# Optimization experiments

Measured on AMD Instinct MI355X. Metric: run time of the kernel, lower is better.

Reference implementation:

```python
import jax, jax.numpy as jnp
import numpy as np

B, LQ, LS, H = 4, 4096, 4096, 1024

def setup_inputs() -> dict:
    key = jax.random.key(0)
    k1, k2 = jax.random.split(key)
    query_input = jax.random.normal(k1, (B, LQ, H), dtype=jnp.float32)
    source_input = jax.random.normal(k2, (B, LS, H), dtype=jnp.float32)
    return {"query_input": query_input, "source_input": source_input}

def reference(query_input, source_input):
    # logits: [B, LQ, LS] = Q @ S^T, scaled by sqrt(d_k)
    dk = jnp.asarray(query_input.shape[-1], dtype=query_input.dtype)
    logits = jnp.einsum('bqh,bsh->bqs', query_input, source_input) / jnp.sqrt(dk)
    weights = jax.nn.softmax(logits, axis=-1)  # dropout inactive in eval mode
    # output: [B, LQ, H] = weights @ S (source doubles as values)
    return jnp.einsum('bqs,bsh->bqh', weights, source_input)
```

## Files before the change

### kernel.cpp

```cpp
#include <hip/hip_runtime.h>
#include <hip/hip_bf16.h>

#define B_   4
#define LQ_  4096
#define LS_  4096
#define DH_  1024
#define BQ_  64
#define BS_  256
#define NT_  (LS_/BS_)
#define NTH  512

typedef __bf16 bf16x8 __attribute__((ext_vector_type(8)));
typedef float  f32x4  __attribute__((ext_vector_type(4)));
typedef float  f32x16 __attribute__((ext_vector_type(16)));
typedef unsigned char u8;

#define WAITL()  asm volatile("s_waitcnt lgkmcnt(0)" ::: "memory")
#define BAR()    __builtin_amdgcn_s_barrier()

__device__ __forceinline__ unsigned short f2bf(float f) {
  union { __bf16 h; unsigned short u; } cv;
  cv.h = (__bf16)f;
  return cv.u;
}
__device__ __forceinline__ bf16x8 cvt8(f32x4 a, f32x4 b) {
  bf16x8 r;
  r[0] = (__bf16)a[0]; r[1] = (__bf16)a[1]; r[2] = (__bf16)a[2]; r[3] = (__bf16)a[3];
  r[4] = (__bf16)b[0]; r[5] = (__bf16)b[1]; r[6] = (__bf16)b[2]; r[7] = (__bf16)b[3];
  return r;
}

__global__ __launch_bounds__(256) void cvt_kernel(const float* __restrict__ S,
                                                  u8* __restrict__ Kf,
                                                  u8* __restrict__ Vf)
{
  __shared__ unsigned short tile[64][72];
  const int b  = blockIdx.z;
  const int dt = blockIdx.y;
  const int st = blockIdx.x;
  const int tid = threadIdx.x;
  const int t  = st >> 2;
  const float* Sbase = S + ((size_t)b*LS_ + (size_t)st*64)*DH_ + dt*64;

  #pragma unroll
  for (int k = 0; k < 4; ++k) {
    int fi  = tid + k*256;
    int row = fi >> 4;
    int c4  = fi & 15;
    float4 v = *reinterpret_cast<const float4*>(Sbase + (size_t)row*DH_ + c4*4);
    ushort4 h;
    h.x = f2bf(v.x); h.y = f2bf(v.y); h.z = f2bf(v.z); h.w = f2bf(v.w);
    *reinterpret_cast<ushort4*>(&tile[row][c4*4]) = h;
  }
  __syncthreads();

  #pragma unroll
  for (int h2 = 0; h2 < 2; ++h2) {
    int u    = tid + h2*256;
    int blk  = u >> 6;
    int wloc = blk >> 2;
    int kkl  = blk & 3;
    int lane = u & 63;
    int sh   = lane >> 5, sl = lane & 31;
    int srow = wloc*32 + sl;
    int scol = kkl*16 + sh*8;
    ushort4 h0 = *reinterpret_cast<const ushort4*>(&tile[srow][scol]);
    ushort4 h1 = *reinterpret_cast<const ushort4*>(&tile[srow][scol+4]);
    int w_g  = (st & 3)*2 + wloc;
    int kk_g = dt*4 + kkl;
    u8* dst = Kf + (size_t)(((b*16 + t)*8 + w_g)*64 + kk_g)*1024 + lane*16;
    *reinterpret_cast<ushort4*>(dst)     = h0;
    *reinterpret_cast<ushort4*>(dst + 8) = h1;
  }

  #pragma unroll
  for (int h2 = 0; h2 < 2; ++h2) {
    int u    = tid + h2*256;
    int blk  = u >> 6;
    int ksl  = blk >> 2;
    int nfl  = blk & 3;
    int lane = u & 63;
    int lg   = lane >> 4, lr = lane & 15;
    int srow = ksl*32 + lg*8;
    int dcol = nfl*16 + lr;
    ushort4 h0, h1;
    h0.x = tile[srow+0][dcol]; h0.y = tile[srow+1][dcol];
    h0.z = tile[srow+2][dcol]; h0.w = tile[srow+3][dcol];
    h1.x = tile[srow+4][dcol]; h1.y = tile[srow+5][dcol];
    h1.z = tile[srow+6][dcol]; h1.w = tile[srow+7][dcol];
    int w_g = dt >> 1;
    int i_g = ((st & 3)*2 + ksl)*8 + (dt & 1)*4 + nfl;
    u8* dst = Vf + (size_t)(((b*16 + t)*8 + w_g)*64 + i_g)*1024 + lane*16;
    *reinterpret_cast<ushort4*>(dst)     = h0;
    *reinterpret_cast<ushort4*>(dst + 8) = h1;
  }
}

__global__ __launch_bounds__(NTH, 1) void attn_kernel(
    const float* __restrict__ Qg,
    const u8* __restrict__ Kf,
    const u8* __restrict__ Vf,
    float* __restrict__ Og)
{
  __shared__ __align__(16) unsigned char qlds[131072];
  __shared__ __align__(16) unsigned char plds[32768];

  const int tid = threadIdx.x;
  const int w  = tid >> 6;
  const int l  = tid & 63;
  const int lg = l >> 4;
  const int lr = l & 15;
  const int sl = l & 31;
  const int sh = l >> 5;

  const int n    = blockIdx.x;
  const int xcd  = n & 7;
  const int slot = n >> 3;
  const int b    = xcd >> 1;
  const int qt   = (xcd & 1)*32 + slot;

  const float* Qbase = Qg + ((size_t)b*LQ_ + (size_t)qt*BQ_)*DH_;
  const u8* kptr = Kf + (size_t)b*8388608 + (size_t)w*65536 + l*16;
  const u8* vptr = Vf + (size_t)b*8388608 + (size_t)w*65536 + l*16;

  bf16x8 bk[4];
  auto ld_bk = [&](int t, int kk) -> bf16x8 {
    return *reinterpret_cast<const bf16x8*>(kptr + (size_t)t*524288 + kk*1024);
  };
  bf16x8 bv[4];
  auto ld_bv = [&](int t, int i) -> bf16x8 {
    return *reinterpret_cast<const bf16x8*>(vptr + (size_t)t*524288 + i*1024);
  };
  auto ldP = [&](int mq, int ks) -> bf16x8 {
    int q = mq*16 + lr;
    return *reinterpret_cast<const bf16x8*>(
        plds + q*512 + ((ks*64 + lg*16) ^ ((q & 7) << 4)));
  };

  bk[0] = ld_bk(0, 0); bk[1] = ld_bk(0, 1); bk[2] = ld_bk(0, 2);

  #pragma unroll
  for (int it = 0; it < 16; ++it) {
    int u  = tid + it*NTH;
    int qf = u >> 12;
    int kk = (u >> 6) & 63;
    int ll = u & 63;
    int q  = qf*32 + (ll & 31);
    int d  = kk*16 + (ll >> 5)*8;
    const float* p = Qbase + (size_t)q*DH_ + d;
    f32x4 v0 = *reinterpret_cast<const f32x4*>(p);
    f32x4 v1 = *reinterpret_cast<const f32x4*>(p + 4);
    *reinterpret_cast<bf16x8*>(qlds + (size_t)u*16) = cvt8(v0, v1);
  }

  f32x4 Oacc[4][8];
  #pragma unroll
  for (int i = 0; i < 4; ++i)
    #pragma unroll
    for (int j = 0; j < 8; ++j)
      Oacc[i][j] = (f32x4){0.f, 0.f, 0.f, 0.f};
  f32x4 lacc[4];
  #pragma unroll
  for (int i = 0; i < 4; ++i) lacc[i] = (f32x4){0.f, 0.f, 0.f, 0.f};

  bf16x8 ones;
  #pragma unroll
  for (int e = 0; e < 8; ++e) ones[e] = (__bf16)1.0f;

  f32x16 qk0, qk1;
  const float SCL = 0.04508422f;

  WAITL();
  BAR();

  #pragma unroll
  for (int r = 0; r < 16; ++r) { qk0[r] = 0.f; qk1[r] = 0.f; }
  {
    bf16x8 aqA0 = *reinterpret_cast<const bf16x8*>(qlds + l*16);
    bf16x8 aqA1 = *reinterpret_cast<const bf16x8*>(qlds + 65536 + l*16);
    #pragma unroll
    for (int kk = 0; kk < 64; ++kk) {
      if (kk < 61) bk[(kk + 3) & 3] = ld_bk(0, kk + 3);
      bf16x8 aqN0, aqN1;
      if (kk < 63) {
        aqN0 = *reinterpret_cast<const bf16x8*>(qlds + (kk + 1)*1024 + l*16);
        aqN1 = *reinterpret_cast<const bf16x8*>(qlds + 65536 + (kk + 1)*1024 + l*16);
      }
      qk0 = __builtin_amdgcn_mfma_f32_32x32x16_bf16(aqA0, bk[kk & 3], qk0, 0, 0, 0);
      qk1 = __builtin_amdgcn_mfma_f32_32x32x16_bf16(aqA1, bk[kk & 3], qk1, 0, 0, 0);
      if (kk < 63) { aqA0 = aqN0; aqA1 = aqN1; }
    }
  }

  for (int t = 1; t < NT_; ++t) {
    BAR();

    #pragma unroll
    for (int r = 0; r < 16; ++r) {
      int qrow = (r & 3) + 8*(r >> 2) + 4*sh;
      int s    = w*32 + sl;
      {
        float p = exp2f(qk0[r] * SCL);
        int q = qrow;
        *reinterpret_cast<__bf16*>(plds + q*512 + ((s*2) ^ ((q & 7) << 4))) = (__bf16)p;
      }
      {
        float p = exp2f(qk1[r] * SCL);
        int q = 32 + qrow;
        *reinterpret_cast<__bf16*>(plds + q*512 + ((s*2) ^ ((q & 7) << 4))) = (__bf16)p;
      }
    }

    bk[0] = ld_bk(t, 0); bk[1] = ld_bk(t, 1); bk[2] = ld_bk(t, 2);
    bv[0] = ld_bv(t-1, 0); bv[1] = ld_bv(t-1, 1); bv[2] = ld_bv(t-1, 2);

    WAITL();
    BAR();

    #pragma unroll
    for (int r = 0; r < 16; ++r) { qk0[r] = 0.f; qk1[r] = 0.f; }

    bf16x8 aqA0 = *reinterpret_cast<const bf16x8*>(qlds + l*16);
    bf16x8 aqA1 = *reinterpret_cast<const bf16x8*>(qlds + 65536 + l*16);
    bf16x8 pa0, pa1, pa2, pa3;

    #pragma unroll
    for (int i = 0; i < 64; ++i) {
      const int ks = i >> 3, nf = i & 7;
      if (i < 61) bk[(i + 3) & 3] = ld_bk(t, i + 3);
      bf16x8 aqN0, aqN1;
      if (i < 63) {
        aqN0 = *reinterpret_cast<const bf16x8*>(qlds + (i + 1)*1024 + l*16);
        aqN1 = *reinterpret_cast<const bf16x8*>(qlds + 65536 + (i + 1)*1024 + l*16);
      }
      qk0 = __builtin_amdgcn_mfma_f32_32x32x16_bf16(aqA0, bk[i & 3], qk0, 0, 0, 0);
      qk1 = __builtin_amdgcn_mfma_f32_32x32x16_bf16(aqA1, bk[i & 3], qk1, 0, 0, 0);
      if (i < 63) { aqA0 = aqN0; aqA1 = aqN1; }

      if (i < 61) bv[(i + 3) & 3] = ld_bv(t-1, i + 3);
      if (nf == 0) {
        pa0 = ldP(0, ks); pa1 = ldP(1, ks); pa2 = ldP(2, ks); pa3 = ldP(3, ks);
        if (w == 0) {
          lacc[0] = __builtin_amdgcn_mfma_f32_16x16x32_bf16(pa0, ones, lacc[0], 0, 0, 0);
          lacc[1] = __builtin_amdgcn_mfma_f32_16x16x32_bf16(pa1, ones, lacc[1], 0, 0, 0);
          lacc[2] = __builtin_amdgcn_mfma_f32_16x16x32_bf16(pa2, ones, lacc[2], 0, 0, 0);
          lacc[3] = __builtin_amdgcn_mfma_f32_16x16x32_bf16(pa3, ones, lacc[3], 0, 0, 0);
        }
      }
      Oacc[0][nf] = __builtin_amdgcn_mfma_f32_16x16x32_bf16(pa0, bv[i & 3], Oacc[0][nf], 0, 0, 0);
      Oacc[1][nf] = __builtin_amdgcn_mfma_f32_16x16x32_bf16(pa1, bv[i & 3], Oacc[1][nf], 0, 0, 0);
      Oacc[2][nf] = __builtin_amdgcn_mfma_f32_16x16x32_bf16(pa2, bv[i & 3], Oacc[2][nf], 0, 0, 0);
      Oacc[3][nf] = __builtin_amdgcn_mfma_f32_16x16x32_bf16(pa3, bv[i & 3], Oacc[3][nf], 0, 0, 0);
    }
  }

  BAR();
  #pragma unroll
  for (int r = 0; r < 16; ++r) {
    int qrow = (r & 3) + 8*(r >> 2) + 4*sh;
    int s    = w*32 + sl;
    {
      float p = exp2f(qk0[r] * SCL);
      int q = qrow;
      *reinterpret_cast<__bf16*>(plds + q*512 + ((s*2) ^ ((q & 7) << 4))) = (__bf16)p;
    }
    {
      float p = exp2f(qk1[r] * SCL);
      int q = 32 + qrow;
      *reinterpret_cast<__bf16*>(plds + q*512 + ((s*2) ^ ((q & 7) << 4))) = (__bf16)p;
    }
  }
  bv[0] = ld_bv(NT_-1, 0); bv[1] = ld_bv(NT_-1, 1); bv[2] = ld_bv(NT_-1, 2);
  WAITL();
  BAR();

  {
    bf16x8 pa0, pa1, pa2, pa3;
    #pragma unroll
    for (int i = 0; i < 64; ++i) {
      const int ks = i >> 3, nf = i & 7;
      if (i < 61) bv[(i + 3) & 3] = ld_bv(NT_-1, i + 3);
      if (nf == 0) {
        pa0 = ldP(0, ks); pa1 = ldP(1, ks); pa2 = ldP(2, ks); pa3 = ldP(3, ks);
        if (w == 0) {
          lacc[0] = __builtin_amdgcn_mfma_f32_16x16x32_bf16(pa0, ones, lacc[0], 0, 0, 0);
          lacc[1] = __builtin_amdgcn_mfma_f32_16x16x32_bf16(pa1, ones, lacc[1], 0, 0, 0);
          lacc[2] = __builtin_amdgcn_mfma_f32_16x16x32_bf16(pa2, ones, lacc[2], 0, 0, 0);
          lacc[3] = __builtin_amdgcn_mfma_f32_16x16x32_bf16(pa3, ones, lacc[3], 0, 0, 0);
        }
      }
      Oacc[0][nf] = __builtin_amdgcn_mfma_f32_16x16x32_bf16(pa0, bv[i & 3], Oacc[0][nf], 0, 0, 0);
      Oacc[1][nf] = __builtin_amdgcn_mfma_f32_16x16x32_bf16(pa1, bv[i & 3], Oacc[1][nf], 0, 0, 0);
      Oacc[2][nf] = __builtin_amdgcn_mfma_f32_16x16x32_bf16(pa2, bv[i & 3], Oacc[2][nf], 0, 0, 0);
      Oacc[3][nf] = __builtin_amdgcn_mfma_f32_16x16x32_bf16(pa3, bv[i & 3], Oacc[3][nf], 0, 0, 0);
    }
  }
  BAR();

  float* lred = (float*)plds;
  if (w == 0 && lr == 0) {
    #pragma unroll
    for (int mq = 0; mq < 4; ++mq)
      #pragma unroll
      for (int j = 0; j < 4; ++j)
        lred[mq*16 + lg*4 + j] = lacc[mq][j];
  }
  WAITL();
  BAR();

  float* Ob = Og + ((size_t)b*LQ_ + (size_t)qt*BQ_)*DH_;
  #pragma unroll
  for (int mq = 0; mq < 4; ++mq)
    #pragma unroll
    for (int j = 0; j < 4; ++j) {
      int q = mq*16 + lg*4 + j;
      float rinv = 1.0f / lred[q];
      #pragma unroll
      for (int nf = 0; nf < 8; ++nf)
        Ob[(size_t)q*DH_ + w*128 + nf*16 + lr] = Oacc[mq][nf][j] * rinv;
    }
}

__global__ void attn_naive(const float* __restrict__ Q, const float* __restrict__ S,
                           float* __restrict__ O)
{
  const int row = blockIdx.x;
  const int b = row >> 12, q = row & 4095;
  const float* qp = Q + ((size_t)b*LQ_ + q)*DH_;
  const float* sp = S + (size_t)b*LS_*DH_;
  __shared__ float qs[DH_];
  __shared__ float osum[DH_];
  __shared__ float lsum;
  for (int i = threadIdx.x; i < DH_; i += 256) { qs[i] = qp[i]; osum[i] = 0.f; }
  if (threadIdx.x == 0) lsum = 0.f;
  __syncthreads();
  float lpart = 0.f;
  for (int s0 = threadIdx.x; s0 < LS_; s0 += 256) {
    const float* sr = sp + (size_t)s0*DH_;
    float dot = 0.f;
    for (int d = 0; d < DH_; ++d) dot += qs[d]*sr[d];
    float p = __expf(dot * 0.03125f);
    lpart += p;
    for (int d = 0; d < DH_; ++d) atomicAdd(&osum[d], p*sr[d]);
  }
  atomicAdd(&lsum, lpart);
  __syncthreads();
  float rinv = 1.0f / lsum;
  float* op = O + ((size_t)b*LQ_ + q)*DH_;
  for (int i = threadIdx.x; i < DH_; i += 256) op[i] = osum[i]*rinv;
}

extern "C" void kernel_launch(void* const* d_in, const int* in_sizes, int n_in,
                              void* d_out, int out_size, void* d_ws, size_t ws_size,
                              hipStream_t stream)
{
  const float* Q = (const float*)d_in[0];
  const float* S = (const float*)d_in[1];
  float* out = (float*)d_out;

  const size_t kf_bytes = (size_t)B_*NT_*8*64*1024;
  const size_t vf_bytes = (size_t)B_*NT_*8*64*1024;
  const size_t need = kf_bytes + vf_bytes;

  if (ws_size >= need) {
    u8* Kf = (u8*)d_ws;
    u8* Vf = Kf + kf_bytes;
    cvt_kernel<<<dim3(64, 16, 4), 256, 0, stream>>>(S, Kf, Vf);
    attn_kernel<<<dim3(256), NTH, 0, stream>>>(Q, Kf, Vf, out);
  } else {
    attn_naive<<<dim3(B_*LQ_), 256, 0, stream>>>(Q, S, out);
  }
}
```

Measured before the change: 347.7 us.

## Stagger K/V chunk order per block and rotate row-sum work across waves

The inner 64-step loops are split into 8 segments of 8. Each block starts at a different segment offset derived from its slot, so concurrent blocks read different parts of K/V at any moment. K/V prefetch now runs continuously across tile boundaries using a 4-deep register rotation, which removes the reload at the start of each tile, and s_setprio is raised around the MFMA groups. The row-sum MFMA work is spread across waves (the wave whose index matches the segment does it) instead of always running on wave 0, with a final cross-wave reduction through LDS. The segment loops use unroll 1, which adds loop overhead and dynamic index math in exchange for smaller code.

```diff
diff --git a/kernel.cpp b/kernel.cpp
--- a/kernel.cpp
+++ b/kernel.cpp
@@ -118,26 +118,27 @@
   const int slot = n >> 3;
   const int b    = xcd >> 1;
   const int qt   = (xcd & 1)*32 + slot;
+  const int off  = slot & 7;
 
   const float* Qbase = Qg + ((size_t)b*LQ_ + (size_t)qt*BQ_)*DH_;
   const u8* kptr = Kf + (size_t)b*8388608 + (size_t)w*65536 + l*16;
   const u8* vptr = Vf + (size_t)b*8388608 + (size_t)w*65536 + l*16;
 
-  bf16x8 bk[4];
-  auto ld_bk = [&](int t, int kk) -> bf16x8 {
-    return *reinterpret_cast<const bf16x8*>(kptr + (size_t)t*524288 + kk*1024);
-  };
-  bf16x8 bv[4];
-  auto ld_bv = [&](int t, int i) -> bf16x8 {
-    return *reinterpret_cast<const bf16x8*>(vptr + (size_t)t*524288 + i*1024);
+  bf16x8 bk[4], bv[4];
+  auto ldU = [&](const u8* base, int unit) -> bf16x8 {
+    return *reinterpret_cast<const bf16x8*>(base + unit*1024);
   };
   auto ldP = [&](int mq, int ks) -> bf16x8 {
     int q = mq*16 + lr;
     return *reinterpret_cast<const bf16x8*>(
         plds + q*512 + ((ks*64 + lg*16) ^ ((q & 7) << 4)));
   };
-
-  bk[0] = ld_bk(0, 0); bk[1] = ld_bk(0, 1); bk[2] = ld_bk(0, 2);
+  auto ldA = [&](int kk, int qf) -> bf16x8 {
+    return *reinterpret_cast<const bf16x8*>(qlds + qf*65536 + kk*1024 + l*16);
+  };
+
+  bk[0] = ldU(kptr, off*8 + 0); bk[1] = ldU(kptr, off*8 + 1);
+  bk[2] = ldU(kptr, off*8 + 2); bk[3] = ldU(kptr, off*8 + 3);
 
   #pragma unroll
   for (int it = 0; it < 16; ++it) {
@@ -173,25 +174,35 @@
   WAITL();
   BAR();
 
+  bf16x8 aqA0 = ldA(off*8, 0);
+  bf16x8 aqA1 = ldA(off*8, 1);
+
   #pragma unroll
   for (int r = 0; r < 16; ++r) { qk0[r] = 0.f; qk1[r] = 0.f; }
-  {
-    bf16x8 aqA0 = *reinterpret_cast<const bf16x8*>(qlds + l*16);
-    bf16x8 aqA1 = *reinterpret_cast<const bf16x8*>(qlds + 65536 + l*16);
-    #pragma unroll
-    for (int kk = 0; kk < 64; ++kk) {
-      if (kk < 61) bk[(kk + 3) & 3] = ld_bk(0, kk + 3);
-      bf16x8 aqN0, aqN1;
-      if (kk < 63) {
-        aqN0 = *reinterpret_cast<const bf16x8*>(qlds + (kk + 1)*1024 + l*16);
-        aqN1 = *reinterpret_cast<const bf16x8*>(qlds + 65536 + (kk + 1)*1024 + l*16);
+  #pragma unroll 1
+  for (int seg = 0; seg < 8; ++seg) {
+    const int ibe = (seg + off) & 7;
+    const int ibn = (ibe + 1) & 7;
+    const u8* kP = (seg < 7) ? kptr : kptr + 524288;
+    #pragma unroll
+    for (int j = 0; j < 8; ++j) {
+      const int nu = (j < 7) ? (ibe*8 + j + 1) : (ibn*8);
+      bf16x8 aqN0 = ldA(nu, 0);
+      bf16x8 aqN1 = ldA(nu, 1);
+      __builtin_amdgcn_s_setprio(1);
+      qk0 = __builtin_amdgcn_mfma_f32_32x32x16_bf16(aqA0, bk[j & 3], qk0, 0, 0, 0);
+      qk1 = __builtin_amdgcn_mfma_f32_32x32x16_bf16(aqA1, bk[j & 3], qk1, 0, 0, 0);
+      __builtin_amdgcn_s_setprio(0);
+      if (j < 4) bk[j] = ldU(kptr, ibe*8 + j + 4);
+      else {
+        bk[j - 4] = ldU(kP, ibn*8 + j - 4);
+        if (seg == 7) bv[j - 4] = ldU(vptr, ibn*8 + j - 4);
       }
-      qk0 = __builtin_amdgcn_mfma_f32_32x32x16_bf16(aqA0, bk[kk & 3], qk0, 0, 0, 0);
-      qk1 = __builtin_amdgcn_mfma_f32_32x32x16_bf16(aqA1, bk[kk & 3], qk1, 0, 0, 0);
-      if (kk < 63) { aqA0 = aqN0; aqA1 = aqN1; }
-    }
-  }
-
+      aqA0 = aqN0; aqA1 = aqN1;
+    }
+  }
+
+  #pragma unroll 1
   for (int t = 1; t < NT_; ++t) {
     BAR();
 
@@ -210,47 +221,53 @@
         *reinterpret_cast<__bf16*>(plds + q*512 + ((s*2) ^ ((q & 7) << 4))) = (__bf16)p;
       }
     }
-
-    bk[0] = ld_bk(t, 0); bk[1] = ld_bk(t, 1); bk[2] = ld_bk(t, 2);
-    bv[0] = ld_bv(t-1, 0); bv[1] = ld_bv(t-1, 1); bv[2] = ld_bv(t-1, 2);
-
     WAITL();
     BAR();
 
     #pragma unroll
     for (int r = 0; r < 16; ++r) { qk0[r] = 0.f; qk1[r] = 0.f; }
 
-    bf16x8 aqA0 = *reinterpret_cast<const bf16x8*>(qlds + l*16);
-    bf16x8 aqA1 = *reinterpret_cast<const bf16x8*>(qlds + 65536 + l*16);
+    const u8* kT = kptr + (size_t)t*524288;
+    const u8* vT = vptr + (size_t)(t-1)*524288;
     bf16x8 pa0, pa1, pa2, pa3;
 
-    #pragma unroll
-    for (int i = 0; i < 64; ++i) {
-      const int ks = i >> 3, nf = i & 7;
-      if (i < 61) bk[(i + 3) & 3] = ld_bk(t, i + 3);
-      bf16x8 aqN0, aqN1;
-      if (i < 63) {
-        aqN0 = *reinterpret_cast<const bf16x8*>(qlds + (i + 1)*1024 + l*16);
-        aqN1 = *reinterpret_cast<const bf16x8*>(qlds + 65536 + (i + 1)*1024 + l*16);
+    #pragma unroll 1
+    for (int seg = 0; seg < 8; ++seg) {
+      const int ibe = (seg + off) & 7;
+      const int ibn = (ibe + 1) & 7;
+      const u8* kP = (seg < 7) ? kT : kT + 524288;
+      const u8* vP = (seg < 7) ? vT : vT + 524288;
+      #pragma unroll
+      for (int j = 0; j < 8; ++j) {
+        const int nu = (j < 7) ? (ibe*8 + j + 1) : (ibn*8);
+        bf16x8 aqN0 = ldA(nu, 0);
+        bf16x8 aqN1 = ldA(nu, 1);
+        if (j == 0) {
+          pa0 = ldP(0, ibe); pa1 = ldP(1, ibe); pa2 = ldP(2, ibe); pa3 = ldP(3, ibe);
+          if (ibe == w) {
+            lacc[0] = __builtin_amdgcn_mfma_f32_16x16x32_bf16(pa0, ones, lacc[0], 0, 0, 0);
+            lacc[1] = __builtin_amdgcn_mfma_f32_16x16x32_bf16(pa1, ones, lacc[1], 0, 0, 0);
+            lacc[2] = __builtin_amdgcn_mfma_f32_16x16x32_bf16(pa2, ones, lacc[2], 0, 0, 0);
+            lacc[3] = __builtin_amdgcn_mfma_f32_16x16x32_bf16(pa3, ones, lacc[3], 0, 0, 0);
+          }
+        }
+        __builtin_amdgcn_s_setprio(1);
+        qk0 = __builtin_amdgcn_mfma_f32_32x32x16_bf16(aqA0, bk[j & 3], qk0, 0, 0, 0);
+        qk1 = __builtin_amdgcn_mfma_f32_32x32x16_bf16(aqA1, bk[j & 3], qk1, 0, 0, 0);
+        Oacc[0][j] = __builtin_amdgcn_mfma_f32_16x16x32_bf16(pa0, bv[j & 3], Oacc[0][j], 0, 0, 0);
+        Oacc[1][j] = __builtin_amdgcn_mfma_f32_16x16x32_bf16(pa1, bv[j & 3], Oacc[1][j], 0, 0, 0);
+        Oacc[2][j] = __builtin_amdgcn_mfma_f32_16x16x32_bf16(pa2, bv[j & 3], Oacc[2][j], 0, 0, 0);
+        Oacc[3][j] = __builtin_amdgcn_mfma_f32_16x16x32_bf16(pa3, bv[j & 3], Oacc[3][j], 0, 0, 0);
+        __builtin_amdgcn_s_setprio(0);
+        if (j < 4) {
+          bk[j] = ldU(kT, ibe*8 + j + 4);
+          bv[j] = ldU(vT, ibe*8 + j + 4);
+        } else {
+          bk[j - 4] = ldU(kP, ibn*8 + j - 4);
+          bv[j - 4] = ldU(vP, ibn*8 + j - 4);
+        }
+        aqA0 = aqN0; aqA1 = aqN1;
       }
-      qk0 = __builtin_amdgcn_mfma_f32_32x32x16_bf16(aqA0, bk[i & 3], qk0, 0, 0, 0);
-      qk1 = __builtin_amdgcn_mfma_f32_32x32x16_bf16(aqA1, bk[i & 3], qk1, 0, 0, 0);
-      if (i < 63) { aqA0 = aqN0; aqA1 = aqN1; }
-
-      if (i < 61) bv[(i + 3) & 3] = ld_bv(t-1, i + 3);
-      if (nf == 0) {
-        pa0 = ldP(0, ks); pa1 = ldP(1, ks); pa2 = ldP(2, ks); pa3 = ldP(3, ks);
-        if (w == 0) {
-          lacc[0] = __builtin_amdgcn_mfma_f32_16x16x32_bf16(pa0, ones, lacc[0], 0, 0, 0);
-          lacc[1] = __builtin_amdgcn_mfma_f32_16x16x32_bf16(pa1, ones, lacc[1], 0, 0, 0);
-          lacc[2] = __builtin_amdgcn_mfma_f32_16x16x32_bf16(pa2, ones, lacc[2], 0, 0, 0);
-          lacc[3] = __builtin_amdgcn_mfma_f32_16x16x32_bf16(pa3, ones, lacc[3], 0, 0, 0);
-        }
-      }
-      Oacc[0][nf] = __builtin_amdgcn_mfma_f32_16x16x32_bf16(pa0, bv[i & 3], Oacc[0][nf], 0, 0, 0);
-      Oacc[1][nf] = __builtin_amdgcn_mfma_f32_16x16x32_bf16(pa1, bv[i & 3], Oacc[1][nf], 0, 0, 0);
-      Oacc[2][nf] = __builtin_amdgcn_mfma_f32_16x16x32_bf16(pa2, bv[i & 3], Oacc[2][nf], 0, 0, 0);
-      Oacc[3][nf] = __builtin_amdgcn_mfma_f32_16x16x32_bf16(pa3, bv[i & 3], Oacc[3][nf], 0, 0, 0);
     }
   }
 
@@ -270,40 +287,47 @@
       *reinterpret_cast<__bf16*>(plds + q*512 + ((s*2) ^ ((q & 7) << 4))) = (__bf16)p;
     }
   }
-  bv[0] = ld_bv(NT_-1, 0); bv[1] = ld_bv(NT_-1, 1); bv[2] = ld_bv(NT_-1, 2);
   WAITL();
   BAR();
 
   {
+    const u8* vT = vptr + (size_t)(NT_-1)*524288;
     bf16x8 pa0, pa1, pa2, pa3;
-    #pragma unroll
-    for (int i = 0; i < 64; ++i) {
-      const int ks = i >> 3, nf = i & 7;
-      if (i < 61) bv[(i + 3) & 3] = ld_bv(NT_-1, i + 3);
-      if (nf == 0) {
-        pa0 = ldP(0, ks); pa1 = ldP(1, ks); pa2 = ldP(2, ks); pa3 = ldP(3, ks);
-        if (w == 0) {
-          lacc[0] = __builtin_amdgcn_mfma_f32_16x16x32_bf16(pa0, ones, lacc[0], 0, 0, 0);
-          lacc[1] = __builtin_amdgcn_mfma_f32_16x16x32_bf16(pa1, ones, lacc[1], 0, 0, 0);
-          lacc[2] = __builtin_amdgcn_mfma_f32_16x16x32_bf16(pa2, ones, lacc[2], 0, 0, 0);
-          lacc[3] = __builtin_amdgcn_mfma_f32_16x16x32_bf16(pa3, ones, lacc[3], 0, 0, 0);
+    #pragma unroll 1
+    for (int seg = 0; seg < 8; ++seg) {
+      const int ibe = (seg + off) & 7;
+      const int ibn = (ibe + 1) & 7;
+      #pragma unroll
+      for (int j = 0; j < 8; ++j) {
+        if (j == 0) {
+          pa0 = ldP(0, ibe); pa1 = ldP(1, ibe); pa2 = ldP(2, ibe); pa3 = ldP(3, ibe);
+          if (ibe == w) {
+            lacc[0] = __builtin_amdgcn_mfma_f32_16x16x32_bf16(pa0, ones, lacc[0], 0, 0, 0);
+            lacc[1] = __builtin_amdgcn_mfma_f32_16x16x32_bf16(pa1, ones, lacc[1], 0, 0, 0);
+            lacc[2] = __builtin_amdgcn_mfma_f32_16x16x32_bf16(pa2, ones, lacc[2], 0, 0, 0);
+            lacc[3] = __builtin_amdgcn_mfma_f32_16x16x32_bf16(pa3, ones, lacc[3], 0, 0, 0);
+          }
         }
+        __builtin_amdgcn_s_setprio(1);
+        Oacc[0][j] = __builtin_amdgcn_mfma_f32_16x16x32_bf16(pa0, bv[j & 3], Oacc[0][j], 0, 0, 0);
+        Oacc[1][j] = __builtin_amdgcn_mfma_f32_16x16x32_bf16(pa1, bv[j & 3], Oacc[1][j], 0, 0, 0);
+        Oacc[2][j] = __builtin_amdgcn_mfma_f32_16x16x32_bf16(pa2, bv[j & 3], Oacc[2][j], 0, 0, 0);
+        Oacc[3][j] = __builtin_amdgcn_mfma_f32_16x16x32_bf16(pa3, bv[j & 3], Oacc[3][j], 0, 0, 0);
+        __builtin_amdgcn_s_setprio(0);
+        if (j < 4)           bv[j] = ldU(vT, ibe*8 + j + 4);
+        else if (seg < 7)    bv[j - 4] = ldU(vT, ibn*8 + j - 4);
       }
-      Oacc[0][nf] = __builtin_amdgcn_mfma_f32_16x16x32_bf16(pa0, bv[i & 3], Oacc[0][nf], 0, 0, 0);
-      Oacc[1][nf] = __builtin_amdgcn_mfma_f32_16x16x32_bf16(pa1, bv[i & 3], Oacc[1][nf], 0, 0, 0);
-      Oacc[2][nf] = __builtin_amdgcn_mfma_f32_16x16x32_bf16(pa2, bv[i & 3], Oacc[2][nf], 0, 0, 0);
-      Oacc[3][nf] = __builtin_amdgcn_mfma_f32_16x16x32_bf16(pa3, bv[i & 3], Oacc[3][nf], 0, 0, 0);
     }
   }
   BAR();
 
   float* lred = (float*)plds;
-  if (w == 0 && lr == 0) {
+  if (lr == 0) {
     #pragma unroll
     for (int mq = 0; mq < 4; ++mq)
       #pragma unroll
       for (int j = 0; j < 4; ++j)
-        lred[mq*16 + lg*4 + j] = lacc[mq][j];
+        lred[w*64 + mq*16 + lg*4 + j] = lacc[mq][j];
   }
   WAITL();
   BAR();
@@ -314,7 +338,10 @@
     #pragma unroll
     for (int j = 0; j < 4; ++j) {
       int q = mq*16 + lg*4 + j;
-      float rinv = 1.0f / lred[q];
+      float s = 0.f;
+      #pragma unroll
+      for (int ww = 0; ww < 8; ++ww) s += lred[ww*64 + q];
+      float rinv = 1.0f / s;
       #pragma unroll
       for (int nf = 0; nf < 8; ++nf)
         Ob[(size_t)q*DH_ + w*128 + nf*16 + lr] = Oacc[mq][nf][j] * rinv;
```

Result: faster. 298.8 us (-14.1%).
